# Kernel tuning notes

Measured on AMD Instinct MI355X. Metric: run time of the kernel, lower is better.

## Reference

```python
import jax, jax.numpy as jnp
import numpy as np

B, T, C = 64, 1024, 32   # batch, seq_len, n_embd
H, D = 4, 8              # num_heads, head_size (H*D == C)


def setup_inputs() -> dict:
    key = jax.random.key(0)
    ks = jax.random.split(key, 6)
    s = 0.02  # init scale for weights
    x = jax.random.normal(ks[0], (B, T, C), dtype=jnp.float32)
    Wq = jax.random.normal(ks[1], (H, C, D), dtype=jnp.float32) * s
    Wk = jax.random.normal(ks[2], (H, C, D), dtype=jnp.float32) * s
    Wv = jax.random.normal(ks[3], (H, C, D), dtype=jnp.float32) * s
    Wproj = jax.random.normal(ks[4], (H * D, C), dtype=jnp.float32) * s
    bproj = jnp.zeros((C,), dtype=jnp.float32)
    return {"x": x, "Wq": Wq, "Wk": Wk, "Wv": Wv, "Wproj": Wproj, "bproj": bproj}


def reference(x, Wq, Wk, Wv, Wproj, bproj):
    # All heads batched into one einsum instead of a Python loop over Head modules.
    q = jnp.einsum('btc,hcd->bhtd', x, Wq)
    k = jnp.einsum('btc,hcd->bhtd', x, Wk)
    v = jnp.einsum('btc,hcd->bhtd', x, Wv)
    scale = D ** -0.5
    att = jnp.einsum('bhtd,bhsd->bhts', q, k) * scale  # [B,H,T,T]
    causal = jnp.tril(jnp.ones((T, T), dtype=bool))
    att = jnp.where(causal, att, jnp.float32(-1e9))
    att = jax.nn.softmax(att, axis=-1)  # dropout omitted (eval mode)
    o = jnp.einsum('bhts,bhsd->bhtd', att, v)
    o = o.transpose(0, 2, 1, 3).reshape(B, T, H * D)  # concat heads on last dim
    return o @ Wproj + bproj  # final proj; output dropout omitted (eval mode)
```

## Files before the change

kernel.cpp:

```cpp
#include <hip/hip_runtime.h>
#include <math.h>

static constexpr int Bb = 64, Tt = 1024, Cc = 32, Hh = 4, Dd = 8;
static constexpr float QSCALE = 0.51006973f;

typedef _Float16 h2  __attribute__((ext_vector_type(2)));
typedef _Float16 v4h __attribute__((ext_vector_type(4)));
typedef float  f32x4 __attribute__((ext_vector_type(4)));

__device__ __forceinline__ h2 pkrtz(float a, float b) {
  return __builtin_bit_cast(h2, __builtin_amdgcn_cvt_pkrtz(a, b));
}

__device__ __forceinline__ float fdot2(h2 a, h2 b, float c) {
#if __has_builtin(__builtin_amdgcn_fdot2)
  return __builtin_amdgcn_fdot2(a, b, c, false);
#else
  return fmaf((float)a.x, (float)b.x, fmaf((float)a.y, (float)b.y, c));
#endif
}

__device__ __forceinline__ float frcp(float x) {
#if __has_builtin(__builtin_amdgcn_rcpf)
  return __builtin_amdgcn_rcpf(x);
#else
  return 1.0f / x;
#endif
}

__device__ __forceinline__ float bperm_f32(int src_lane, float v) {
  return __builtin_bit_cast(float,
      __builtin_amdgcn_ds_bpermute(src_lane << 2, __builtin_bit_cast(int, v)));
}

__device__ __forceinline__ h2 exp2h2(h2 s) {
  const h2 A3 = {(_Float16)0.05550411f, (_Float16)0.05550411f};
  const h2 A2 = {(_Float16)0.24022651f, (_Float16)0.24022651f};
  const h2 A1 = {(_Float16)0.69314718f, (_Float16)0.69314718f};
  const h2 ONE = {(_Float16)1.0f, (_Float16)1.0f};
  h2 t = A3 * s + A2;
  t = t * s + A1;
  t = t * s + ONE;
  return t;
}

union U4 { uint4 u; h2 h[4]; };
union P2 { uint2 u; h2 h[2]; v4h v; };

__device__ __forceinline__ void chain_step(const P2& ak, const v4h& bv,
                                           const P2& bq, f32x4& o) {
  const f32x4 zero4 = {0.f, 0.f, 0.f, 0.f};
  f32x4 s = __builtin_amdgcn_mfma_f32_16x16x16f16(ak.v, bq.v, zero4, 0, 0, 0);
  h2 p0 = exp2h2(pkrtz(s[0], s[1]));
  h2 p1 = exp2h2(pkrtz(s[2], s[3]));
  P2 pf; pf.h[0] = p0; pf.h[1] = p1;
  o = __builtin_amdgcn_mfma_f32_16x16x16f16(pf.v, bv, o, 0, 0, 0);
}

__device__ __forceinline__ void chain_step_masked(const P2& ak, const v4h& bv,
                                                  const P2& bq, f32x4& o,
                                                  h2 km0, h2 km1) {
  const f32x4 zero4 = {0.f, 0.f, 0.f, 0.f};
  f32x4 s = __builtin_amdgcn_mfma_f32_16x16x16f16(ak.v, bq.v, zero4, 0, 0, 0);
  h2 p0 = exp2h2(pkrtz(s[0], s[1])) * km0;
  h2 p1 = exp2h2(pkrtz(s[2], s[3])) * km1;
  P2 pf; pf.h[0] = p0; pf.h[1] = p1;
  o = __builtin_amdgcn_mfma_f32_16x16x16f16(pf.v, bv, o, 0, 0, 0);
}

__global__ __launch_bounds__(512, 4) void fused_attn_kernel(
    const float* __restrict__ x, const float* __restrict__ Wq,
    const float* __restrict__ Wk, const float* __restrict__ Wv,
    ushort* __restrict__ og)
{
  __shared__ h2 wT[3][Dd][16];
  __shared__ __align__(16) ushort ks[Tt * Dd];
  __shared__ __align__(16) ushort vs[9 * 1032];
  __shared__ __align__(16) ushort qs[Tt * Dd];

  const int tid = threadIdx.x;
  const int bh = blockIdx.x & 255;
  const int g  = blockIdx.x >> 8;
  const int b = bh >> 2, h = bh & 3;

  if (tid < 384) {
    const int mat = tid >> 7, d = (tid >> 4) & 7, c2 = tid & 15;
    const float* W = (mat == 0) ? Wq : (mat == 1) ? Wk : Wv;
    const float w0 = W[(h * Cc + 2 * c2) * Dd + d];
    const float w1 = W[(h * Cc + 2 * c2 + 1) * Dd + d];
    wT[mat][d][c2] = pkrtz(w0, w1);
  } else {
    const int i = tid - 384;
    const unsigned one2 = 0x3C003C00u;
    *(uint4*)(vs + 8 * 1032 + i * 8) = make_uint4(one2, one2, one2, one2);
  }

  const int t0 = tid, t1 = tid + 512;
  h2 xa[16], xb[16];
  {
    const float4* g0 = (const float4*)(x + ((long)b * Tt + t0) * Cc);
    const float4* g1 = (const float4*)(x + ((long)b * Tt + t1) * Cc);
#pragma unroll
    for (int i = 0; i < 8; ++i) {
      float4 va = g0[i], vb = g1[i];
      xa[2 * i]     = pkrtz(va.x, va.y);
      xa[2 * i + 1] = pkrtz(va.z, va.w);
      xb[2 * i]     = pkrtz(vb.x, vb.y);
      xb[2 * i + 1] = pkrtz(vb.z, vb.w);
    }
  }
  __syncthreads();

#pragma unroll
  for (int mat = 0; mat < 3; ++mat) {
    float a0[Dd], a1[Dd];
#pragma unroll
    for (int d = 0; d < Dd; ++d) {
      float s0 = 0.f, s1 = 0.f;
#pragma unroll
      for (int c2 = 0; c2 < 16; ++c2) {
        const h2 w = wT[mat][d][c2];
        s0 = fdot2(xa[c2], w, s0);
        s1 = fdot2(xb[c2], w, s1);
      }
      a0[d] = s0; a1[d] = s1;
    }
    if (mat == 2) {
#pragma unroll
      for (int d = 0; d < Dd; ++d) {
        ((_Float16*)vs)[d * 1032 + t0] = (_Float16)a0[d];
        ((_Float16*)vs)[d * 1032 + t1] = (_Float16)a1[d];
      }
    } else {
      const float sc = (mat == 0) ? QSCALE : 1.0f;
      ushort* dst = (mat == 0) ? qs : ks;
      U4 u0, u1;
#pragma unroll
      for (int i = 0; i < 4; ++i) {
        u0.h[i] = pkrtz(a0[2 * i] * sc, a0[2 * i + 1] * sc);
        u1.h[i] = pkrtz(a1[2 * i] * sc, a1[2 * i + 1] * sc);
      }
      ((uint4*)(dst + t0 * Dd))[0] = u0.u;
      ((uint4*)(dst + t1 * Dd))[0] = u1.u;
    }
  }
  __syncthreads();

  const int lane = tid & 63;
  const int u  = __builtin_amdgcn_readfirstlane(tid >> 6);
  const int w  = g * 8 + u;
  int rb[4];
  rb[0] = w; rb[1] = 31 - w; rb[2] = 32 + w; rb[3] = 63 - w;

  const int n = lane & 15, quad = lane >> 4;
  const ushort* kbase = ks + n * Dd + (quad & 1) * 4;
  const int vr = (n <= 8) ? n : (n - 8);
  const ushort* vbase = vs + vr * 1032 + quad * 4;

  const h2 km0 = {(_Float16)((4 * quad + 0) <= n ? 1.f : 0.f),
                  (_Float16)((4 * quad + 1) <= n ? 1.f : 0.f)};
  const h2 km1 = {(_Float16)((4 * quad + 2) <= n ? 1.f : 0.f),
                  (_Float16)((4 * quad + 3) <= n ? 1.f : 0.f)};

  P2 bq[4];
#pragma unroll
  for (int i = 0; i < 4; ++i) {
    uint2 r = *(const uint2*)(qs + (rb[i] * 16 + n) * Dd + (quad & 1) * 4);
    if (quad & 2) { r.x = 0; r.y = 0; }
    bq[i].u = r;
  }

  const f32x4 zero4 = {0.f, 0.f, 0.f, 0.f};
  f32x4 o[4];
#pragma unroll
  for (int i = 0; i < 4; ++i) o[i] = zero4;

#define LOAD_AKBV                                         \
  P2 ak; ak.u = *(const uint2*)(kbase + ct * 128);        \
  const v4h bv = *(const v4h*)(vbase + ct * 16);

  int ct = 0;
#pragma unroll 2
  for (; ct < rb[0]; ++ct) {
    LOAD_AKBV;
    chain_step(ak, bv, bq[0], o[0]);
    chain_step(ak, bv, bq[1], o[1]);
    chain_step(ak, bv, bq[2], o[2]);
    chain_step(ak, bv, bq[3], o[3]);
  }
  {
    LOAD_AKBV;
    chain_step_masked(ak, bv, bq[0], o[0], km0, km1);
    chain_step(ak, bv, bq[1], o[1]);
    chain_step(ak, bv, bq[2], o[2]);
    chain_step(ak, bv, bq[3], o[3]);
    ++ct;
  }
#pragma unroll 2
  for (; ct < rb[1]; ++ct) {
    LOAD_AKBV;
    chain_step(ak, bv, bq[1], o[1]);
    chain_step(ak, bv, bq[2], o[2]);
    chain_step(ak, bv, bq[3], o[3]);
  }
  {
    LOAD_AKBV;
    chain_step_masked(ak, bv, bq[1], o[1], km0, km1);
    chain_step(ak, bv, bq[2], o[2]);
    chain_step(ak, bv, bq[3], o[3]);
    ++ct;
  }
#pragma unroll 2
  for (; ct < rb[2]; ++ct) {
    LOAD_AKBV;
    chain_step(ak, bv, bq[2], o[2]);
    chain_step(ak, bv, bq[3], o[3]);
  }
  {
    LOAD_AKBV;
    chain_step_masked(ak, bv, bq[2], o[2], km0, km1);
    chain_step(ak, bv, bq[3], o[3]);
    ++ct;
  }
#pragma unroll 2
  for (; ct < rb[3]; ++ct) {
    LOAD_AKBV;
    chain_step(ak, bv, bq[3], o[3]);
  }
  {
    LOAD_AKBV;
    chain_step_masked(ak, bv, bq[3], o[3], km0, km1);
  }
#undef LOAD_AKBV

  const int lsrc = (lane & 48) | 8;
#pragma unroll
  for (int i = 0; i < 4; ++i) {
#pragma unroll
    for (int r = 0; r < 4; ++r) {
      const float l = bperm_f32(lsrc, o[i][r]);
      const float ov = o[i][r] * frcp(l);
      if (n < 8) {
        const int q = rb[i] * 16 + 4 * quad + r;
        ((_Float16*)og)[(((long)b * Tt + q) * Hh + h) * Dd + n] = (_Float16)ov;
      }
    }
  }
}

__global__ __launch_bounds__(256) void proj_kernel(
    const ushort* __restrict__ o_ws, const float* __restrict__ Wp,
    const float* __restrict__ bp, float* __restrict__ out)
{
  __shared__ h2 wT[Cc][16];
  __shared__ float bps[Cc];
  const int tid = threadIdx.x;
  {
    const int c = tid & 31, hp = tid >> 5;
#pragma unroll
    for (int i = 0; i < 2; ++i) {
      const int hd2 = hp + 8 * i;
      wT[c][hd2] = pkrtz(Wp[(2 * hd2) * Cc + c], Wp[(2 * hd2 + 1) * Cc + c]);
    }
    if (tid < Cc) bps[tid] = bp[tid];
  }
  __syncthreads();

  const int bt = blockIdx.x * 256 + tid;
  h2 orow[16];
  {
    const uint4* op = (const uint4*)(o_ws + (long)bt * Cc);
#pragma unroll
    for (int w = 0; w < 4; ++w) {
      U4 uu; uu.u = op[w];
#pragma unroll
      for (int i = 0; i < 4; ++i) orow[w * 4 + i] = uu.h[i];
    }
  }
  float acc[Cc];
#pragma unroll
  for (int c = 0; c < Cc; ++c) {
    float a = bps[c];
#pragma unroll
    for (int hd2 = 0; hd2 < 16; ++hd2) a = fdot2(orow[hd2], wT[c][hd2], a);
    acc[c] = a;
  }
  float4* og2 = (float4*)(out + (long)bt * Cc);
#pragma unroll
  for (int c4 = 0; c4 < 8; ++c4)
    og2[c4] = make_float4(acc[c4 * 4], acc[c4 * 4 + 1], acc[c4 * 4 + 2], acc[c4 * 4 + 3]);
}

extern "C" void kernel_launch(void* const* d_in, const int* in_sizes, int n_in,
                              void* d_out, int out_size, void* d_ws, size_t ws_size,
                              hipStream_t stream) {
  const float* x  = (const float*)d_in[0];
  const float* Wq = (const float*)d_in[1];
  const float* Wk = (const float*)d_in[2];
  const float* Wv = (const float*)d_in[3];
  const float* Wp = (const float*)d_in[4];
  const float* bp = (const float*)d_in[5];
  float* out = (float*)d_out;

  ushort* o_ws = (ushort*)d_ws;

  fused_attn_kernel<<<Bb * Hh * 2, 512, 0, stream>>>(x, Wq, Wk, Wv, o_ws);
  proj_kernel<<<Bb * Tt / 256, 256, 0, stream>>>(o_ws, Wp, bp, out);
}
```

Before: 107.9 us.

## Split attention work into four blocks per batch-head with two row-blocks per wave

The grid doubles to four blocks per (batch, head), and each wave now handles two causal-balanced 16-row query blocks instead of four. The QKV projection is recomputed per block, one token at a time in a non-unrolled loop, and only the query rows a block needs are kept in a smaller shared buffer. Launch bounds rise to 8 waves per SIMD so more blocks can be resident. This exposes more parallelism and shortens each wave's serial MFMA chain, at the cost of recomputing K/V projections twice as often and tighter register limits.

```diff
diff --git a/kernel.cpp b/kernel.cpp
--- a/kernel.cpp
+++ b/kernel.cpp
@@ -68,7 +68,7 @@
   o = __builtin_amdgcn_mfma_f32_16x16x16f16(pf.v, bv, o, 0, 0, 0);
 }
 
-__global__ __launch_bounds__(512, 4) void fused_attn_kernel(
+__global__ __launch_bounds__(512, 8) void fused_attn_kernel(
     const float* __restrict__ x, const float* __restrict__ Wq,
     const float* __restrict__ Wk, const float* __restrict__ Wv,
     ushort* __restrict__ og)
@@ -76,7 +76,7 @@
   __shared__ h2 wT[3][Dd][16];
   __shared__ __align__(16) ushort ks[Tt * Dd];
   __shared__ __align__(16) ushort vs[9 * 1032];
-  __shared__ __align__(16) ushort qs[Tt * Dd];
+  __shared__ __align__(16) ushort qsm[256 * Dd];
 
   const int tid = threadIdx.x;
   const int bh = blockIdx.x & 255;
@@ -94,54 +94,55 @@
     const unsigned one2 = 0x3C003C00u;
     *(uint4*)(vs + 8 * 1032 + i * 8) = make_uint4(one2, one2, one2, one2);
   }
-
-  const int t0 = tid, t1 = tid + 512;
-  h2 xa[16], xb[16];
-  {
-    const float4* g0 = (const float4*)(x + ((long)b * Tt + t0) * Cc);
-    const float4* g1 = (const float4*)(x + ((long)b * Tt + t1) * Cc);
-#pragma unroll
-    for (int i = 0; i < 8; ++i) {
-      float4 va = g0[i], vb = g1[i];
-      xa[2 * i]     = pkrtz(va.x, va.y);
-      xa[2 * i + 1] = pkrtz(va.z, va.w);
-      xb[2 * i]     = pkrtz(vb.x, vb.y);
-      xb[2 * i + 1] = pkrtz(vb.z, vb.w);
-    }
-  }
   __syncthreads();
 
-#pragma unroll
-  for (int mat = 0; mat < 3; ++mat) {
-    float a0[Dd], a1[Dd];
-#pragma unroll
-    for (int d = 0; d < Dd; ++d) {
-      float s0 = 0.f, s1 = 0.f;
-#pragma unroll
-      for (int c2 = 0; c2 < 16; ++c2) {
-        const h2 w = wT[mat][d][c2];
-        s0 = fdot2(xa[c2], w, s0);
-        s1 = fdot2(xb[c2], w, s1);
-      }
-      a0[d] = s0; a1[d] = s1;
-    }
-    if (mat == 2) {
+#pragma unroll 1
+  for (int it = 0; it < 2; ++it) {
+    const int t = tid + 512 * it;
+    h2 xr[16];
+    {
+      const float4* gx = (const float4*)(x + ((long)b * Tt + t) * Cc);
+#pragma unroll
+      for (int i = 0; i < 8; ++i) {
+        float4 v = gx[i];
+        xr[2 * i]     = pkrtz(v.x, v.y);
+        xr[2 * i + 1] = pkrtz(v.z, v.w);
+      }
+    }
+#pragma unroll
+    for (int mat = 0; mat < 3; ++mat) {
+      float a[Dd];
 #pragma unroll
       for (int d = 0; d < Dd; ++d) {
-        ((_Float16*)vs)[d * 1032 + t0] = (_Float16)a0[d];
-        ((_Float16*)vs)[d * 1032 + t1] = (_Float16)a1[d];
-      }
-    } else {
-      const float sc = (mat == 0) ? QSCALE : 1.0f;
-      ushort* dst = (mat == 0) ? qs : ks;
-      U4 u0, u1;
-#pragma unroll
-      for (int i = 0; i < 4; ++i) {
-        u0.h[i] = pkrtz(a0[2 * i] * sc, a0[2 * i + 1] * sc);
-        u1.h[i] = pkrtz(a1[2 * i] * sc, a1[2 * i + 1] * sc);
-      }
-      ((uint4*)(dst + t0 * Dd))[0] = u0.u;
-      ((uint4*)(dst + t1 * Dd))[0] = u1.u;
+        float s = 0.f;
+#pragma unroll
+        for (int c2 = 0; c2 < 16; ++c2) s = fdot2(xr[c2], wT[mat][d][c2], s);
+        a[d] = s;
+      }
+      if (mat == 0) {
+        const int blk16 = t >> 4;
+        const int r1 = blk16 - 8 * g;
+        const int r2 = blk16 - (56 - 8 * g);
+        int idx = -1;
+        if ((unsigned)r1 < 8u) idx = r1 * 16 + (t & 15);
+        else if ((unsigned)r2 < 8u) idx = 128 + r2 * 16 + (t & 15);
+        if (idx >= 0) {
+          U4 uq;
+#pragma unroll
+          for (int i = 0; i < 4; ++i)
+            uq.h[i] = pkrtz(a[2 * i] * QSCALE, a[2 * i + 1] * QSCALE);
+          ((uint4*)(qsm + idx * Dd))[0] = uq.u;
+        }
+      } else if (mat == 1) {
+        U4 uk;
+#pragma unroll
+        for (int i = 0; i < 4; ++i) uk.h[i] = pkrtz(a[2 * i], a[2 * i + 1]);
+        ((uint4*)(ks + t * Dd))[0] = uk.u;
+      } else {
+#pragma unroll
+        for (int d = 0; d < Dd; ++d)
+          ((_Float16*)vs)[d * 1032 + t] = (_Float16)a[d];
+      }
     }
   }
   __syncthreads();
@@ -149,8 +150,7 @@
   const int lane = tid & 63;
   const int u  = __builtin_amdgcn_readfirstlane(tid >> 6);
   const int w  = g * 8 + u;
-  int rb[4];
-  rb[0] = w; rb[1] = 31 - w; rb[2] = 32 + w; rb[3] = 63 - w;
+  const int rb0 = w, rb1 = 63 - w;
 
   const int n = lane & 15, quad = lane >> 4;
   const ushort* kbase = ks + n * Dd + (quad & 1) * 4;
@@ -162,18 +162,18 @@
   const h2 km1 = {(_Float16)((4 * quad + 2) <= n ? 1.f : 0.f),
                   (_Float16)((4 * quad + 3) <= n ? 1.f : 0.f)};
 
-  P2 bq[4];
-#pragma unroll
-  for (int i = 0; i < 4; ++i) {
-    uint2 r = *(const uint2*)(qs + (rb[i] * 16 + n) * Dd + (quad & 1) * 4);
-    if (quad & 2) { r.x = 0; r.y = 0; }
-    bq[i].u = r;
+  P2 bq[2];
+  {
+    const int i0 = u * 16 + n;
+    const int i1 = 128 + (7 - u) * 16 + n;
+    uint2 r0 = *(const uint2*)(qsm + i0 * Dd + (quad & 1) * 4);
+    uint2 r1 = *(const uint2*)(qsm + i1 * Dd + (quad & 1) * 4);
+    if (quad & 2) { r0.x = 0; r0.y = 0; r1.x = 0; r1.y = 0; }
+    bq[0].u = r0; bq[1].u = r1;
   }
 
   const f32x4 zero4 = {0.f, 0.f, 0.f, 0.f};
-  f32x4 o[4];
-#pragma unroll
-  for (int i = 0; i < 4; ++i) o[i] = zero4;
+  f32x4 o[2] = {zero4, zero4};
 
 #define LOAD_AKBV                                         \
   P2 ak; ak.u = *(const uint2*)(kbase + ct * 128);        \
@@ -181,67 +181,38 @@
 
   int ct = 0;
 #pragma unroll 2
-  for (; ct < rb[0]; ++ct) {
+  for (; ct < rb0; ++ct) {
     LOAD_AKBV;
     chain_step(ak, bv, bq[0], o[0]);
     chain_step(ak, bv, bq[1], o[1]);
-    chain_step(ak, bv, bq[2], o[2]);
-    chain_step(ak, bv, bq[3], o[3]);
   }
   {
     LOAD_AKBV;
     chain_step_masked(ak, bv, bq[0], o[0], km0, km1);
     chain_step(ak, bv, bq[1], o[1]);
-    chain_step(ak, bv, bq[2], o[2]);
-    chain_step(ak, bv, bq[3], o[3]);
     ++ct;
   }
 #pragma unroll 2
-  for (; ct < rb[1]; ++ct) {
+  for (; ct < rb1; ++ct) {
     LOAD_AKBV;
     chain_step(ak, bv, bq[1], o[1]);
-    chain_step(ak, bv, bq[2], o[2]);
-    chain_step(ak, bv, bq[3], o[3]);
   }
   {
     LOAD_AKBV;
     chain_step_masked(ak, bv, bq[1], o[1], km0, km1);
-    chain_step(ak, bv, bq[2], o[2]);
-    chain_step(ak, bv, bq[3], o[3]);
-    ++ct;
-  }
-#pragma unroll 2
-  for (; ct < rb[2]; ++ct) {
-    LOAD_AKBV;
-    chain_step(ak, bv, bq[2], o[2]);
-    chain_step(ak, bv, bq[3], o[3]);
-  }
-  {
-    LOAD_AKBV;
-    chain_step_masked(ak, bv, bq[2], o[2], km0, km1);
-    chain_step(ak, bv, bq[3], o[3]);
-    ++ct;
-  }
-#pragma unroll 2
-  for (; ct < rb[3]; ++ct) {
-    LOAD_AKBV;
-    chain_step(ak, bv, bq[3], o[3]);
-  }
-  {
-    LOAD_AKBV;
-    chain_step_masked(ak, bv, bq[3], o[3], km0, km1);
   }
 #undef LOAD_AKBV
 
   const int lsrc = (lane & 48) | 8;
-#pragma unroll
-  for (int i = 0; i < 4; ++i) {
+  const int rbs[2] = {rb0, rb1};
+#pragma unroll
+  for (int i = 0; i < 2; ++i) {
 #pragma unroll
     for (int r = 0; r < 4; ++r) {
       const float l = bperm_f32(lsrc, o[i][r]);
       const float ov = o[i][r] * frcp(l);
       if (n < 8) {
-        const int q = rb[i] * 16 + 4 * quad + r;
+        const int q = rbs[i] * 16 + 4 * quad + r;
         ((_Float16*)og)[(((long)b * Tt + q) * Hh + h) * Dd + n] = (_Float16)ov;
       }
     }
@@ -304,6 +275,6 @@
 
   ushort* o_ws = (ushort*)d_ws;
 
-  fused_attn_kernel<<<Bb * Hh * 2, 512, 0, stream>>>(x, Wq, Wk, Wv, o_ws);
+  fused_attn_kernel<<<Bb * Hh * 4, 512, 0, stream>>>(x, Wq, Wk, Wv, o_ws);
   proj_kernel<<<Bb * Tt / 256, 256, 0, stream>>>(o_ws, Wp, bp, out);
 }
```

Measured after the change: 368.0 us. +241.2%, slower.
